# Kernel tuning notes

Hardware: AMD Instinct MI355X
Metric: run time of the kernel (lower is better)

Reference implementation:

```python
import jax, jax.numpy as jnp
import numpy as np

B, L, D, H = 4, 2048, 512, 8
HD = D // H
NEG = -1e9


def setup_inputs() -> dict:
    key = jax.random.key(0)
    ks = jax.random.split(key, 11)
    s = 1.0 / np.sqrt(D)
    inp = {
        "q": jax.random.normal(ks[0], (B, L, D), jnp.float32),
        "k": jax.random.normal(ks[1], (B, L, D), jnp.float32),
        "v": jax.random.normal(ks[2], (B, L, D), jnp.float32),
        "mask": jnp.broadcast_to(jnp.tril(jnp.ones((L, L), jnp.int32)), (B, L, L)),
        "Wq": jax.random.normal(ks[3], (D, D), jnp.float32) * s,
        "bq": jax.random.normal(ks[4], (D,), jnp.float32) * s,
        "Wk": jax.random.normal(ks[5], (D, D), jnp.float32) * s,
        "bk": jax.random.normal(ks[6], (D,), jnp.float32) * s,
        "Wv": jax.random.normal(ks[7], (D, D), jnp.float32) * s,
        "bv": jax.random.normal(ks[8], (D,), jnp.float32) * s,
        "Wo": jax.random.normal(ks[9], (D, D), jnp.float32) * s,
        "bo": jax.random.normal(ks[10], (D,), jnp.float32) * s,
    }
    return inp


def reference(q, k, v, mask, Wq, bq, Wk, bk, Wv, bv, Wo, bo):
    # Linear projections (torch Linear: x @ W.T + b)
    Q = (q @ Wq.T + bq).reshape(B, L, H, HD).transpose(0, 2, 1, 3)  # [B,H,L,hd]
    K = (k @ Wk.T + bk).reshape(B, L, H, HD).transpose(0, 2, 1, 3)
    V = (v @ Wv.T + bv).reshape(B, L, H, HD).transpose(0, 2, 1, 3)
    # scaled dot-product attention with masked_fill(mask==0, -1e9)
    score = jnp.einsum('bhqd,bhkd->bhqk', Q, K) / jnp.sqrt(jnp.float32(HD))
    score = jnp.where(mask[:, None, :, :] == 0, NEG, score)
    attn = jax.nn.softmax(score, axis=-1)
    ctx = jnp.einsum('bhqk,bhkd->bhqd', attn, V)  # [B,H,L,hd]
    ctx = ctx.transpose(0, 2, 1, 3).reshape(B, L, D)
    return ctx @ Wo.T + bo
```

## Files before the change

kernel.cpp:

```cpp
#include <hip/hip_runtime.h>
#include <hip/hip_bf16.h>
#include <math.h>

constexpr int Bc  = 4;
constexpr int Lc  = 2048;
constexpr int Dc  = 512;
constexpr int Hc  = 8;
constexpr int HDc = 64;

constexpr int GK = Dc;
constexpr int BK = 64;

typedef __attribute__((ext_vector_type(8))) short bf16x8;
typedef __attribute__((ext_vector_type(4))) short bf16x4;
typedef __attribute__((ext_vector_type(4))) float f32x4;
typedef __attribute__((ext_vector_type(16))) float f32x16;
typedef __attribute__((ext_vector_type(4))) int i32x4;

static __device__ __forceinline__ short f2bf(float x) {
    __hip_bfloat16 h = __float2bfloat16(x);
    return (short)__builtin_bit_cast(unsigned short, h);
}

static __device__ __forceinline__ int cvtpk_bf16(float lo, float hi) {
    int r;
    asm("v_cvt_pk_bf16_f32 %0, %1, %2" : "=v"(r) : "v"(lo), "v"(hi));
    return r;
}

static __device__ __forceinline__ void gload_lds16(const void* g, void* l) {
    __builtin_amdgcn_global_load_lds(
        (const __attribute__((address_space(1))) void*)g,
        (__attribute__((address_space(3))) void*)l, 16, 0, 0);
}

__global__ __launch_bounds__(256)
void cast_all(const float* __restrict__ q, const float* __restrict__ k,
              const float* __restrict__ v, const float* __restrict__ wq,
              const float* __restrict__ wk, const float* __restrict__ wv,
              const float* __restrict__ wo, short* __restrict__ dst) {
    const size_t i = ((size_t)blockIdx.x * 256 + threadIdx.x) * 8;
    const float* src; size_t off;
    if      (i <  4194304) { src = q;  off = i; }
    else if (i <  8388608) { src = k;  off = i -  4194304; }
    else if (i < 12582912) { src = v;  off = i -  8388608; }
    else if (i < 12845056) { src = wq; off = i - 12582912; }
    else if (i < 13107200) { src = wk; off = i - 12845056; }
    else if (i < 13369344) { src = wv; off = i - 13107200; }
    else                   { src = wo; off = i - 13369344; }
    const float4 a = *(const float4*)(src + off);
    const float4 b = *(const float4*)(src + off + 4);
    bf16x8 o;
    o[0] = f2bf(a.x); o[1] = f2bf(a.y); o[2] = f2bf(a.z); o[3] = f2bf(a.w);
    o[4] = f2bf(b.x); o[5] = f2bf(b.y); o[6] = f2bf(b.z); o[7] = f2bf(b.w);
    *(bf16x8*)(dst + i) = o;
}

template<int BM, int BN, int WMT, int WNT>
__device__ __forceinline__ void gemm_tile(const short* __restrict__ A,
                                          const short* __restrict__ W,
                                          short* As, short* Bs,
                                          f32x4 (&acc)[WMT][WNT],
                                          int m0, int n0) {
    const int tid  = threadIdx.x;
    const int w    = tid >> 6;
    const int lane = tid & 63;
    const int low4 = lane & 15;
    const int quad = lane >> 4;
    const int wm   = w & 1, wn = w >> 1;
    const int lrow = lane >> 3;
    const int lchk = (lane & 7) * 8;

    for (int k0 = 0; k0 < GK; k0 += BK) {
#pragma unroll
        for (int i = 0; i < BM / 32; ++i) {
            const int r0 = i * 32 + w * 8;
            gload_lds16(A + (size_t)(m0 + r0 + lrow) * GK + k0 + lchk, As + r0 * BK);
        }
#pragma unroll
        for (int i = 0; i < BN / 32; ++i) {
            const int r0 = i * 32 + w * 8;
            gload_lds16(W + (size_t)(n0 + r0 + lrow) * GK + k0 + lchk, Bs + r0 * BK);
        }
        __syncthreads();
#pragma unroll
        for (int ks = 0; ks < 2; ++ks) {
            bf16x8 af[WMT], bfr[WNT];
#pragma unroll
            for (int mi = 0; mi < WMT; ++mi)
                af[mi] = *(const bf16x8*)(As + (wm * WMT * 16 + mi * 16 + low4) * BK + ks * 32 + quad * 8);
#pragma unroll
            for (int ni = 0; ni < WNT; ++ni)
                bfr[ni] = *(const bf16x8*)(Bs + (wn * WNT * 16 + ni * 16 + low4) * BK + ks * 32 + quad * 8);
#pragma unroll
            for (int mi = 0; mi < WMT; ++mi)
#pragma unroll
                for (int ni = 0; ni < WNT; ++ni)
                    acc[mi][ni] = __builtin_amdgcn_mfma_f32_16x16x32_bf16(af[mi], bfr[ni], acc[mi][ni], 0, 0, 0);
        }
        __syncthreads();
    }
}

__global__ __launch_bounds__(256)
void qkv_gemm(const short* __restrict__ Xq, const short* __restrict__ Xk,
              const short* __restrict__ Xv, const short* __restrict__ Wcat,
              const float* __restrict__ bq, const float* __restrict__ bk,
              const float* __restrict__ bv,
              short* __restrict__ Qw, short* __restrict__ Kw, short* __restrict__ Vw) {
    __shared__ __align__(16) short Smem[128 * 138];
    short* As = Smem;
    short* Bs = Smem + 8192;
    short* Ts = Smem;

    const int tid = threadIdx.x;
    const int i    = blockIdx.x;
    const int slot = i >> 3;
    const int g    = (i & 7) + 8 * (slot >> 2);
    const int j    = slot & 3;
    const int z    = g >> 6;
    const int m0   = (g & 63) * 128;
    const int n0   = z * 512 + j * 128;

    const short* A    = (z == 0) ? Xq : (z == 1) ? Xk : Xv;
    const float* bias = (z == 0) ? bq : (z == 1) ? bk : bv;

    f32x4 acc[4][4];
#pragma unroll
    for (int mi = 0; mi < 4; ++mi)
#pragma unroll
        for (int ni = 0; ni < 4; ++ni) acc[mi][ni] = (f32x4){0.f, 0.f, 0.f, 0.f};

    gemm_tile<128, 128, 4, 4>(A, Wcat, As, Bs, acc, m0, n0);

    const int lane = tid & 63, w = tid >> 6;
    const int low4 = lane & 15, quad = lane >> 4;
    const int wm = w & 1, wn = w >> 1;

    if (z < 2) {
        short* Y = (z == 0) ? Qw : Kw;
#pragma unroll
        for (int mi = 0; mi < 4; ++mi)
#pragma unroll
            for (int ni = 0; ni < 4; ++ni)
#pragma unroll
                for (int r = 0; r < 4; ++r) {
                    const int rowL = wm * 64 + mi * 16 + quad * 4 + r;
                    const int colL = wn * 64 + ni * 16 + low4;
                    const int c    = (n0 & 511) + colL;
                    Ts[rowL * 138 + colL] = f2bf(acc[mi][ni][r] + bias[c]);
                }
        __syncthreads();
        const int jj = tid & 7;
        const int b = m0 >> 11;
#pragma unroll
        for (int it = 0; it < 8; ++it) {
            const int slot2 = it * 32 + (tid >> 3);
            const int row  = slot2 >> 1, half = slot2 & 1;
            const int c0 = (n0 & 511) + half * 64;
            const int h  = c0 >> 6;
            const int l  = (m0 & 2047) + row;
            short* dst = Y + (((size_t)b * Hc + h) * Lc + l) * HDc + jj * 8;
            *(bf16x8*)dst = *(const bf16x8*)(Ts + row * 138 + half * 64 + jj * 8);
        }
    } else {
#pragma unroll
        for (int mi = 0; mi < 4; ++mi)
#pragma unroll
            for (int ni = 0; ni < 4; ++ni)
#pragma unroll
                for (int r = 0; r < 4; ++r) {
                    const int rowL = wm * 64 + mi * 16 + quad * 4 + r;
                    const int colL = wn * 64 + ni * 16 + low4;
                    const int c    = (n0 + colL) & 511;
                    Ts[colL * 136 + rowL] = f2bf(acc[mi][ni][r] + bias[c]);
                }
        __syncthreads();
        const int hdl = tid >> 1, seg = tid & 1;
        const int c  = (n0 + hdl) & 511;
        const int h  = c >> 6, hd = c & 63;
        const int b  = m0 >> 11, l0 = (m0 & 2047) + seg * 64;
        short* dst = Vw + (((size_t)b * Hc + h) * HDc + hd) * Lc + l0;
        const short* srcT = Ts + hdl * 136 + seg * 64;
#pragma unroll
        for (int jj = 0; jj < 8; ++jj)
            *(bf16x8*)(dst + jj * 8) = *(const bf16x8*)(srcT + jj * 8);
    }
}

__global__ __launch_bounds__(256)
void out_gemm(const short* __restrict__ A, const short* __restrict__ W,
              const float* __restrict__ bias, float* __restrict__ Y) {
    __shared__ __align__(16) float SmemF[64 * 132];
    short* As = (short*)SmemF;
    short* Bs = As + 64 * BK;
    float* Tf = SmemF;

    const int tid = threadIdx.x;
    const int i    = blockIdx.x;
    const int slot = i >> 3;
    const int g    = (i & 7) + 8 * (slot >> 2);
    const int j    = slot & 3;
    const int m0   = g * 64;
    const int n0   = j * 128;

    f32x4 acc[2][4];
#pragma unroll
    for (int mi = 0; mi < 2; ++mi)
#pragma unroll
        for (int ni = 0; ni < 4; ++ni) acc[mi][ni] = (f32x4){0.f, 0.f, 0.f, 0.f};

    gemm_tile<64, 128, 2, 4>(A, W, As, Bs, acc, m0, n0);

    const int lane = tid & 63, w = tid >> 6;
    const int low4 = lane & 15, quad = lane >> 4;
    const int wm = w & 1, wn = w >> 1;
#pragma unroll
    for (int mi = 0; mi < 2; ++mi)
#pragma unroll
        for (int ni = 0; ni < 4; ++ni)
#pragma unroll
            for (int r = 0; r < 4; ++r) {
                const int rowL = wm * 32 + mi * 16 + quad * 4 + r;
                const int colL = wn * 64 + ni * 16 + low4;
                Tf[rowL * 132 + colL] = acc[mi][ni][r] + bias[n0 + colL];
            }
    __syncthreads();

    const int c = (tid & 31) * 4;
#pragma unroll
    for (int p = 0; p < 8; ++p) {
        const int row = p * 8 + (tid >> 5);
        *(float4*)(Y + (size_t)(m0 + row) * Dc + n0 + c) =
            *(const float4*)(Tf + row * 132 + c);
    }
}

__global__ __launch_bounds__(256, 2)
void flash_attn(const short* __restrict__ Qb, const short* __restrict__ Kb,
                const short* __restrict__ VTb, short* __restrict__ ctx) {
    __shared__ __align__(16) short Kf[3][4096];
    __shared__ __align__(16) short Vf[3][4096];
    __shared__ __align__(16) float Cb[2][64 * 36];
    __shared__ float Cl[2][64];

    const int tid  = threadIdx.x;
    const int w    = tid >> 6;
    const int lane = tid & 63;
    const int t31  = lane & 31;
    const int hh   = lane >> 5;
    const int x7   = t31 & 7;
    const int qcol = w & 1;
    const int kh   = w >> 1;

    const int u  = blockIdx.x;
    const int bh = u & 31;
    const int pm = u >> 5;

    const short* Qg = Qb  + (size_t)bh * Lc * HDc;
    const short* Kg = Kb  + (size_t)bh * Lc * HDc;
    const short* Vg = VTb + (size_t)bh * HDc * Lc;

    const int grow = lane >> 3;
    const int gcol = ((lane & 7) ^ grow) * 8;

    const float C8 = 0.18033688f;
    const int bb = bh >> 3, head = bh & 7;
    short* cg = ctx + (size_t)bb * Lc * Dc + (size_t)head * HDc;

#define STAGE(KT_, BUF_)                                                       \
    {                                                                          \
        _Pragma("unroll")                                                      \
        for (int p = 0; p < 2; ++p) {                                          \
            const int ii = w + 4 * p;                                          \
            gload_lds16(Kg + (size_t)((KT_) + ii * 8 + grow) * HDc + gcol,     \
                        &Kf[BUF_][ii * 512]);                                  \
            gload_lds16(Vg + (size_t)(ii * 8 + grow) * Lc + (KT_) + gcol,      \
                        &Vf[BUF_][ii * 512]);                                  \
        }                                                                      \
    }

    auto run_part = [&](int a) {
        const int n  = a + 1;
        const int q0 = a * 64 + qcol * 32;

        bf16x8 qa[4];
#pragma unroll
        for (int hc = 0; hc < 4; ++hc)
            qa[hc] = *(const bf16x8*)(Qg + (size_t)(q0 + t31) * HDc + hc * 16 + hh * 8);

        STAGE(0, 0);
        if (n > 1) {
            STAGE(64, 1);
            asm volatile("s_waitcnt vmcnt(4)" ::: "memory");
        } else {
            asm volatile("s_waitcnt vmcnt(0)" ::: "memory");
        }
        __builtin_amdgcn_sched_barrier(0);
        __builtin_amdgcn_s_barrier();

        f32x16 o0, o1;
#pragma unroll
        for (int i = 0; i < 16; ++i) { o0[i] = 0.f; o1[i] = 0.f; }
        float lps = 0.f;
        int br = 0;

        for (int t = 0; t < n; ++t) {
            const int bs = (br + 2 >= 3) ? br - 1 : br + 2;
            if (t + 2 < n) STAGE((t + 2) * 64, bs);

            const bool lastT = (t == a);
            if (!(lastT && qcol == 0 && kh == 1)) {
                f32x16 s;
#pragma unroll
                for (int i = 0; i < 16; ++i) s[i] = 0.f;
                const short* kfb = Kf[br];
#pragma unroll
                for (int hc = 0; hc < 4; ++hc) {
                    const int cb = ((hc * 2 + hh) ^ x7) << 3;
                    const bf16x8 kfr = *(const bf16x8*)(kfb + (kh * 32 + t31) * 64 + cb);
                    s = __builtin_amdgcn_mfma_f32_32x32x16_bf16(kfr, qa[hc], s, 0, 0, 0);
                }

                if (lastT && !(qcol == 1 && kh == 0)) {
                    const int qv  = q0 + t31;
                    const int kb0 = t * 64 + kh * 32 + 4 * hh;
#pragma unroll
                    for (int r = 0; r < 16; ++r) {
                        const int kl = kb0 + (r & 3) + 8 * (r >> 2);
                        const float p = (kl <= qv) ? exp2f(s[r] * C8) : 0.f;
                        lps += p; s[r] = p;
                    }
                } else {
#pragma unroll
                    for (int r = 0; r < 16; ++r) {
                        const float p = exp2f(s[r] * C8);
                        lps += p; s[r] = p;
                    }
                }

                const short* vfb = Vf[br];
#pragma unroll
                for (int kc = 0; kc < 2; ++kc) {
                    const int g = 8 * kc;
                    int u0 = cvtpk_bf16(s[g],     s[g + 1]);
                    int u1 = cvtpk_bf16(s[g + 2], s[g + 3]);
                    int v0 = cvtpk_bf16(s[g + 4], s[g + 5]);
                    int v1 = cvtpk_bf16(s[g + 6], s[g + 7]);
                    asm volatile("v_permlane32_swap_b32 %0, %1" : "+v"(u0), "+v"(v0));
                    asm volatile("v_permlane32_swap_b32 %0, %1" : "+v"(u1), "+v"(v1));
                    i32x4 pw; pw[0] = u0; pw[1] = u1; pw[2] = v0; pw[3] = v1;
                    const bf16x8 pa = __builtin_bit_cast(bf16x8, pw);

                    const int cbv = ((kh * 4 + kc * 2 + hh) ^ x7) << 3;
                    const bf16x8 vf0 = *(const bf16x8*)(vfb + t31 * 64 + cbv);
                    const bf16x8 vf1 = *(const bf16x8*)(vfb + (32 + t31) * 64 + cbv);
                    o0 = __builtin_amdgcn_mfma_f32_32x32x16_bf16(pa, vf0, o0, 0, 0, 0);
                    o1 = __builtin_amdgcn_mfma_f32_32x32x16_bf16(pa, vf1, o1, 0, 0, 0);
                }
            }

            if (t + 2 < n) asm volatile("s_waitcnt vmcnt(4)" ::: "memory");
            else           asm volatile("s_waitcnt vmcnt(0)" ::: "memory");
            __builtin_amdgcn_sched_barrier(0);
            __builtin_amdgcn_s_barrier();
            br = (br + 1 >= 3) ? 0 : br + 1;
        }

        lps += __shfl_xor(lps, 32, 64);

        if (kh == 1) {
#pragma unroll
            for (int j = 0; j < 4; ++j) {
                f32x4 a0 = {o0[4 * j], o0[4 * j + 1], o0[4 * j + 2], o0[4 * j + 3]};
                f32x4 a1 = {o1[4 * j], o1[4 * j + 1], o1[4 * j + 2], o1[4 * j + 3]};
                *(f32x4*)&Cb[qcol][lane * 36 + j * 4]      = a0;
                *(f32x4*)&Cb[qcol][lane * 36 + 16 + j * 4] = a1;
            }
            Cl[qcol][lane] = lps;
        }
        __syncthreads();
        if (kh == 0) {
            lps += Cl[qcol][lane];
#pragma unroll
            for (int j = 0; j < 4; ++j) {
                const f32x4 a0 = *(const f32x4*)&Cb[qcol][lane * 36 + j * 4];
                const f32x4 a1 = *(const f32x4*)&Cb[qcol][lane * 36 + 16 + j * 4];
#pragma unroll
                for (int e = 0; e < 4; ++e) {
                    o0[4 * j + e] += a0[e];
                    o1[4 * j + e] += a1[e];
                }
            }
            const float inv = 1.f / lps;
#pragma unroll
            for (int r = 0; r < 16; ++r) {
                const int qloc = (r & 3) + 8 * (r >> 2) + 4 * hh;
                const float iq = __shfl(inv, qloc, 64);
                short* row = cg + (size_t)(q0 - qcol * 32 + qcol * 32 + qloc) * Dc;
                row[t31]      = f2bf(o0[r] * iq);
                row[32 + t31] = f2bf(o1[r] * iq);
            }
        }
        __syncthreads();
    };

    run_part(31 - pm);
    run_part(pm);
#undef STAGE
}

extern "C" void kernel_launch(void* const* d_in, const int* in_sizes, int n_in,
                              void* d_out, int out_size, void* d_ws, size_t ws_size,
                              hipStream_t stream) {
    const float* q  = (const float*)d_in[0];
    const float* k  = (const float*)d_in[1];
    const float* v  = (const float*)d_in[2];
    const float* Wq = (const float*)d_in[4];
    const float* bq = (const float*)d_in[5];
    const float* Wk = (const float*)d_in[6];
    const float* bk = (const float*)d_in[7];
    const float* Wv = (const float*)d_in[8];
    const float* bv = (const float*)d_in[9];
    const float* Wo = (const float*)d_in[10];
    const float* bo = (const float*)d_in[11];
    float* out = (float*)d_out;

    const size_t per = (size_t)Bc * Lc * Dc;
    const size_t wsz = (size_t)Dc * Dc;
    short* Xq   = (short*)d_ws;
    short* Xk   = Xq + per;
    short* Xv   = Xk + per;
    short* Wcat = Xv + per;
    short* Wob  = Wcat + 3 * wsz;
    short* Qw   = Wob + wsz;
    short* Kw   = Qw + per;
    short* Vw   = Kw + per;
    short* Cw   = Vw + per;

    cast_all<<<6656, 256, 0, stream>>>(q, k, v, Wq, Wk, Wv, Wo, Xq);

    qkv_gemm<<<768, 256, 0, stream>>>(Xq, Xk, Xv, Wcat,
                                      bq, bk, bv, Qw, Kw, Vw);

    flash_attn<<<512, 256, 0, stream>>>(Qw, Kw, Vw, Cw);

    out_gemm<<<512, 256, 0, stream>>>(Cw, Wob, bo, out);
}
```

Before: 228.0 us.

## Split paired causal tiles into separate blocks and double-buffer at higher occupancy

Each flash-attention block previously handled a heavy and a light 64-row query tile in sequence. Now each block handles one tile, so the grid doubles to 1024 blocks and heavy tiles are scheduled first. The K/V staging drops from triple to double buffering, and the cross-wave reduction buffers reuse the K/V LDS arrays. Together these cut shared memory so launch bounds can request 4 blocks per CU. The softmax scale (log2e/sqrt(hd)) is folded into Q in the projection epilogue, which removes a multiply per score but gives a shallower prefetch pipeline with a full vmcnt(0) wait each iteration.

```diff
diff --git a/kernel.cpp b/kernel.cpp
--- a/kernel.cpp
+++ b/kernel.cpp
@@ -139,6 +139,7 @@
 
     if (z < 2) {
         short* Y = (z == 0) ? Qw : Kw;
+        const float qs = (z == 0) ? 0.18033688f : 1.0f;
 #pragma unroll
         for (int mi = 0; mi < 4; ++mi)
 #pragma unroll
@@ -148,7 +149,7 @@
                     const int rowL = wm * 64 + mi * 16 + quad * 4 + r;
                     const int colL = wn * 64 + ni * 16 + low4;
                     const int c    = (n0 & 511) + colL;
-                    Ts[rowL * 138 + colL] = f2bf(acc[mi][ni][r] + bias[c]);
+                    Ts[rowL * 138 + colL] = f2bf((acc[mi][ni][r] + bias[c]) * qs);
                 }
         __syncthreads();
         const int jj = tid & 7;
@@ -236,13 +237,11 @@
     }
 }
 
-__global__ __launch_bounds__(256, 2)
+__global__ __launch_bounds__(256, 4)
 void flash_attn(const short* __restrict__ Qb, const short* __restrict__ Kb,
                 const short* __restrict__ VTb, short* __restrict__ ctx) {
-    __shared__ __align__(16) short Kf[3][4096];
-    __shared__ __align__(16) short Vf[3][4096];
-    __shared__ __align__(16) float Cb[2][64 * 36];
-    __shared__ float Cl[2][64];
+    __shared__ __align__(16) short Kf[2][4096];
+    __shared__ __align__(16) short Vf[2][4096];
 
     const int tid  = threadIdx.x;
     const int w    = tid >> 6;
@@ -255,7 +254,10 @@
 
     const int u  = blockIdx.x;
     const int bh = u & 31;
-    const int pm = u >> 5;
+    const int j  = u >> 5;
+    const int a  = (j < 16) ? (31 - j) : (j - 16);
+    const int n  = a + 1;
+    const int q0 = a * 64 + qcol * 32;
 
     const short* Qg = Qb  + (size_t)bh * Lc * HDc;
     const short* Kg = Kb  + (size_t)bh * Lc * HDc;
@@ -264,7 +266,6 @@
     const int grow = lane >> 3;
     const int gcol = ((lane & 7) ^ grow) * 8;
 
-    const float C8 = 0.18033688f;
     const int bb = bh >> 3, head = bh & 7;
     short* cg = ctx + (size_t)bb * Lc * Dc + (size_t)head * HDc;
 
@@ -280,133 +281,119 @@
         }                                                                      \
     }
 
-    auto run_part = [&](int a) {
-        const int n  = a + 1;
-        const int q0 = a * 64 + qcol * 32;
-
-        bf16x8 qa[4];
-#pragma unroll
-        for (int hc = 0; hc < 4; ++hc)
-            qa[hc] = *(const bf16x8*)(Qg + (size_t)(q0 + t31) * HDc + hc * 16 + hh * 8);
-
-        STAGE(0, 0);
-        if (n > 1) {
-            STAGE(64, 1);
-            asm volatile("s_waitcnt vmcnt(4)" ::: "memory");
-        } else {
-            asm volatile("s_waitcnt vmcnt(0)" ::: "memory");
-        }
+    bf16x8 qa[4];
+#pragma unroll
+    for (int hc = 0; hc < 4; ++hc)
+        qa[hc] = *(const bf16x8*)(Qg + (size_t)(q0 + t31) * HDc + hc * 16 + hh * 8);
+
+    STAGE(0, 0);
+    asm volatile("s_waitcnt vmcnt(0)" ::: "memory");
+    __builtin_amdgcn_sched_barrier(0);
+    __builtin_amdgcn_s_barrier();
+
+    f32x16 o0, o1;
+#pragma unroll
+    for (int i = 0; i < 16; ++i) { o0[i] = 0.f; o1[i] = 0.f; }
+    float lps = 0.f;
+
+    for (int t = 0; t < n; ++t) {
+        const int buf = t & 1;
+        if (t + 1 < n) STAGE((t + 1) * 64, buf ^ 1);
+
+        const bool lastT = (t == a);
+        if (!(lastT && qcol == 0 && kh == 1)) {
+            f32x16 s;
+#pragma unroll
+            for (int i = 0; i < 16; ++i) s[i] = 0.f;
+            const short* kfb = Kf[buf];
+#pragma unroll
+            for (int hc = 0; hc < 4; ++hc) {
+                const int cb = ((hc * 2 + hh) ^ x7) << 3;
+                const bf16x8 kfr = *(const bf16x8*)(kfb + (kh * 32 + t31) * 64 + cb);
+                s = __builtin_amdgcn_mfma_f32_32x32x16_bf16(kfr, qa[hc], s, 0, 0, 0);
+            }
+
+            if (lastT && !(qcol == 1 && kh == 0)) {
+                const int qv  = q0 + t31;
+                const int kb0 = t * 64 + kh * 32 + 4 * hh;
+#pragma unroll
+                for (int r = 0; r < 16; ++r) {
+                    const int kl = kb0 + (r & 3) + 8 * (r >> 2);
+                    const float p = (kl <= qv) ? exp2f(s[r]) : 0.f;
+                    lps += p; s[r] = p;
+                }
+            } else {
+#pragma unroll
+                for (int r = 0; r < 16; ++r) {
+                    const float p = exp2f(s[r]);
+                    lps += p; s[r] = p;
+                }
+            }
+
+            const short* vfb = Vf[buf];
+#pragma unroll
+            for (int kc = 0; kc < 2; ++kc) {
+                const int g = 8 * kc;
+                int u0 = cvtpk_bf16(s[g],     s[g + 1]);
+                int u1 = cvtpk_bf16(s[g + 2], s[g + 3]);
+                int v0 = cvtpk_bf16(s[g + 4], s[g + 5]);
+                int v1 = cvtpk_bf16(s[g + 6], s[g + 7]);
+                asm volatile("v_permlane32_swap_b32 %0, %1" : "+v"(u0), "+v"(v0));
+                asm volatile("v_permlane32_swap_b32 %0, %1" : "+v"(u1), "+v"(v1));
+                i32x4 pw; pw[0] = u0; pw[1] = u1; pw[2] = v0; pw[3] = v1;
+                const bf16x8 pa = __builtin_bit_cast(bf16x8, pw);
+
+                const int cbv = ((kh * 4 + kc * 2 + hh) ^ x7) << 3;
+                const bf16x8 vf0 = *(const bf16x8*)(vfb + t31 * 64 + cbv);
+                const bf16x8 vf1 = *(const bf16x8*)(vfb + (32 + t31) * 64 + cbv);
+                o0 = __builtin_amdgcn_mfma_f32_32x32x16_bf16(pa, vf0, o0, 0, 0, 0);
+                o1 = __builtin_amdgcn_mfma_f32_32x32x16_bf16(pa, vf1, o1, 0, 0, 0);
+            }
+        }
+
+        asm volatile("s_waitcnt vmcnt(0)" ::: "memory");
         __builtin_amdgcn_sched_barrier(0);
         __builtin_amdgcn_s_barrier();
-
-        f32x16 o0, o1;
-#pragma unroll
-        for (int i = 0; i < 16; ++i) { o0[i] = 0.f; o1[i] = 0.f; }
-        float lps = 0.f;
-        int br = 0;
-
-        for (int t = 0; t < n; ++t) {
-            const int bs = (br + 2 >= 3) ? br - 1 : br + 2;
-            if (t + 2 < n) STAGE((t + 2) * 64, bs);
-
-            const bool lastT = (t == a);
-            if (!(lastT && qcol == 0 && kh == 1)) {
-                f32x16 s;
-#pragma unroll
-                for (int i = 0; i < 16; ++i) s[i] = 0.f;
-                const short* kfb = Kf[br];
-#pragma unroll
-                for (int hc = 0; hc < 4; ++hc) {
-                    const int cb = ((hc * 2 + hh) ^ x7) << 3;
-                    const bf16x8 kfr = *(const bf16x8*)(kfb + (kh * 32 + t31) * 64 + cb);
-                    s = __builtin_amdgcn_mfma_f32_32x32x16_bf16(kfr, qa[hc], s, 0, 0, 0);
-                }
-
-                if (lastT && !(qcol == 1 && kh == 0)) {
-                    const int qv  = q0 + t31;
-                    const int kb0 = t * 64 + kh * 32 + 4 * hh;
-#pragma unroll
-                    for (int r = 0; r < 16; ++r) {
-                        const int kl = kb0 + (r & 3) + 8 * (r >> 2);
-                        const float p = (kl <= qv) ? exp2f(s[r] * C8) : 0.f;
-                        lps += p; s[r] = p;
-                    }
-                } else {
-#pragma unroll
-                    for (int r = 0; r < 16; ++r) {
-                        const float p = exp2f(s[r] * C8);
-                        lps += p; s[r] = p;
-                    }
-                }
-
-                const short* vfb = Vf[br];
-#pragma unroll
-                for (int kc = 0; kc < 2; ++kc) {
-                    const int g = 8 * kc;
-                    int u0 = cvtpk_bf16(s[g],     s[g + 1]);
-                    int u1 = cvtpk_bf16(s[g + 2], s[g + 3]);
-                    int v0 = cvtpk_bf16(s[g + 4], s[g + 5]);
-                    int v1 = cvtpk_bf16(s[g + 6], s[g + 7]);
-                    asm volatile("v_permlane32_swap_b32 %0, %1" : "+v"(u0), "+v"(v0));
-                    asm volatile("v_permlane32_swap_b32 %0, %1" : "+v"(u1), "+v"(v1));
-                    i32x4 pw; pw[0] = u0; pw[1] = u1; pw[2] = v0; pw[3] = v1;
-                    const bf16x8 pa = __builtin_bit_cast(bf16x8, pw);
-
-                    const int cbv = ((kh * 4 + kc * 2 + hh) ^ x7) << 3;
-                    const bf16x8 vf0 = *(const bf16x8*)(vfb + t31 * 64 + cbv);
-                    const bf16x8 vf1 = *(const bf16x8*)(vfb + (32 + t31) * 64 + cbv);
-                    o0 = __builtin_amdgcn_mfma_f32_32x32x16_bf16(pa, vf0, o0, 0, 0, 0);
-                    o1 = __builtin_amdgcn_mfma_f32_32x32x16_bf16(pa, vf1, o1, 0, 0, 0);
-                }
+    }
+
+    lps += __shfl_xor(lps, 32, 64);
+
+    float* CbX = (qcol == 0) ? (float*)&Kf[1][0] : (float*)&Vf[1][0];
+    float* ClX = (float*)&Kf[0][0] + qcol * 64;
+
+    if (kh == 1) {
+#pragma unroll
+        for (int jj = 0; jj < 4; ++jj) {
+            f32x4 a0 = {o0[4 * jj], o0[4 * jj + 1], o0[4 * jj + 2], o0[4 * jj + 3]};
+            f32x4 a1 = {o1[4 * jj], o1[4 * jj + 1], o1[4 * jj + 2], o1[4 * jj + 3]};
+            *(f32x4*)&CbX[lane * 32 + jj * 4]      = a0;
+            *(f32x4*)&CbX[lane * 32 + 16 + jj * 4] = a1;
+        }
+        ClX[lane] = lps;
+    }
+    __syncthreads();
+    if (kh == 0) {
+        lps += ClX[lane];
+#pragma unroll
+        for (int jj = 0; jj < 4; ++jj) {
+            const f32x4 a0 = *(const f32x4*)&CbX[lane * 32 + jj * 4];
+            const f32x4 a1 = *(const f32x4*)&CbX[lane * 32 + 16 + jj * 4];
+#pragma unroll
+            for (int e = 0; e < 4; ++e) {
+                o0[4 * jj + e] += a0[e];
+                o1[4 * jj + e] += a1[e];
             }
-
-            if (t + 2 < n) asm volatile("s_waitcnt vmcnt(4)" ::: "memory");
-            else           asm volatile("s_waitcnt vmcnt(0)" ::: "memory");
-            __builtin_amdgcn_sched_barrier(0);
-            __builtin_amdgcn_s_barrier();
-            br = (br + 1 >= 3) ? 0 : br + 1;
-        }
-
-        lps += __shfl_xor(lps, 32, 64);
-
-        if (kh == 1) {
-#pragma unroll
-            for (int j = 0; j < 4; ++j) {
-                f32x4 a0 = {o0[4 * j], o0[4 * j + 1], o0[4 * j + 2], o0[4 * j + 3]};
-                f32x4 a1 = {o1[4 * j], o1[4 * j + 1], o1[4 * j + 2], o1[4 * j + 3]};
-                *(f32x4*)&Cb[qcol][lane * 36 + j * 4]      = a0;
-                *(f32x4*)&Cb[qcol][lane * 36 + 16 + j * 4] = a1;
-            }
-            Cl[qcol][lane] = lps;
-        }
-        __syncthreads();
-        if (kh == 0) {
-            lps += Cl[qcol][lane];
-#pragma unroll
-            for (int j = 0; j < 4; ++j) {
-                const f32x4 a0 = *(const f32x4*)&Cb[qcol][lane * 36 + j * 4];
-                const f32x4 a1 = *(const f32x4*)&Cb[qcol][lane * 36 + 16 + j * 4];
-#pragma unroll
-                for (int e = 0; e < 4; ++e) {
-                    o0[4 * j + e] += a0[e];
-                    o1[4 * j + e] += a1[e];
-                }
-            }
-            const float inv = 1.f / lps;
-#pragma unroll
-            for (int r = 0; r < 16; ++r) {
-                const int qloc = (r & 3) + 8 * (r >> 2) + 4 * hh;
-                const float iq = __shfl(inv, qloc, 64);
-                short* row = cg + (size_t)(q0 - qcol * 32 + qcol * 32 + qloc) * Dc;
-                row[t31]      = f2bf(o0[r] * iq);
-                row[32 + t31] = f2bf(o1[r] * iq);
-            }
-        }
-        __syncthreads();
-    };
-
-    run_part(31 - pm);
-    run_part(pm);
+        }
+        const float inv = 1.f / lps;
+#pragma unroll
+        for (int r = 0; r < 16; ++r) {
+            const int qloc = (r & 3) + 8 * (r >> 2) + 4 * hh;
+            const float iq = __shfl(inv, qloc, 64);
+            short* row = cg + (size_t)(q0 + qloc) * Dc;
+            row[t31]      = f2bf(o0[r] * iq);
+            row[32 + t31] = f2bf(o1[r] * iq);
+        }
+    }
 #undef STAGE
 }
 
@@ -443,7 +430,7 @@
     qkv_gemm<<<768, 256, 0, stream>>>(Xq, Xk, Xv, Wcat,
                                       bq, bk, bv, Qw, Kw, Vw);
 
-    flash_attn<<<512, 256, 0, stream>>>(Qw, Kw, Vw, Cw);
+    flash_attn<<<1024, 256, 0, stream>>>(Qw, Kw, Vw, Cw);
 
     out_gemm<<<512, 256, 0, stream>>>(Cw, Wob, bo, out);
 }
```

After: 223.0 us. 2.2% less time.
